# Kernel tuning notes

Measured on AMD Instinct MI355X. Metric: run time of the kernel, lower is better.

The kernel has to match this reference:

```python
import jax, jax.numpy as jnp
import numpy as np

N, D, R, E = 10000, 1024, 8, 80000


def setup_inputs() -> dict:
    key = jax.random.key(0)
    ks = jax.random.split(key, 8)
    s = 1.0 / np.sqrt(D)
    x = jax.random.normal(ks[0], (N, D), dtype=jnp.float32)
    edge_index = jax.random.randint(ks[1], (2, E), 0, N, dtype=jnp.int64)
    edge_type = jax.random.randint(ks[2], (E,), 0, R, dtype=jnp.int64)
    weight = jax.random.normal(ks[3], (R, D, D), dtype=jnp.float32) * s  # per-relation W_r
    root = jax.random.normal(ks[4], (D, D), dtype=jnp.float32) * s      # root/self-loop weight
    bias = jnp.zeros((D,), dtype=jnp.float32)
    w_gate = jax.random.normal(ks[5], (2 * D, D), dtype=jnp.float32) * (1.0 / np.sqrt(2 * D))
    b_gate = jnp.zeros((D,), dtype=jnp.float32)
    return {"x": x, "edge_index": edge_index, "edge_type": edge_type,
            "weight": weight, "root": root, "bias": bias,
            "w_gate": w_gate, "b_gate": b_gate}


def _rgcn(x, edge_index, edge_type, weight, root, bias):
    # PyG RGCNConv (aggr='mean'): per relation r, mean-aggregate x[src] into dst,
    # then transform by W_r (aggregate-then-transform, equivalent by linearity).
    src, dst = edge_index[0], edge_index[1]
    msgs = x[src]                                   # [E, D] gather
    out = x @ root + bias                           # root/self connection
    n = x.shape[0]
    for r in range(weight.shape[0]):                # small fixed relation loop
        mask = (edge_type == r).astype(x.dtype)     # [E]
        sums = jax.ops.segment_sum(msgs * mask[:, None], dst, num_segments=n)
        cnt = jax.ops.segment_sum(mask, dst, num_segments=n)
        mean = sums / jnp.maximum(cnt, 1.0)[:, None]
        out = out + mean @ weight[r]
    return out


def reference(x, edge_index, edge_type, weight, root, bias, w_gate, b_gate):
    u = _rgcn(x, edge_index, edge_type, weight, root, bias)
    # dropout p=0 -> identity
    z = jnp.concatenate([u, x], axis=1) @ w_gate + b_gate
    h = jnp.tanh(u) * z + x * (1.0 - z)
    return h
```

## Files before the change

### kernel.cpp

```cpp
#include <hip/hip_runtime.h>
#include <math.h>

typedef unsigned short u16;
typedef __attribute__((ext_vector_type(8))) short bf16x8;
typedef __attribute__((ext_vector_type(4))) float f32x4;

static constexpr int kN = 10000;
static constexpr int kNpad = 10240;
static constexpr int kD = 1024;
static constexpr int kR = 8;
static constexpr int kE = 80000;
static constexpr int kKz = 2 * kD;
static constexpr int kCrows = kNpad * (kR + 1);
static constexpr int kTilesY1 = kCrows / 128;

#define GLB(p) ((const __attribute__((address_space(1))) unsigned int*)(const void*)(p))
#define LDSP(p) ((__attribute__((address_space(3))) unsigned int*)(p))

__device__ __forceinline__ u16 f2bf(float f) {
    union { float f; unsigned int i; } c; c.f = f;
    unsigned int u = c.i;
    return (u16)((u + 0x7FFFu + ((u >> 16) & 1u)) >> 16);
}
__device__ __forceinline__ float bf2f(u16 u) {
    union { unsigned int i; float f; } c; c.i = ((unsigned int)u) << 16;
    return c.f;
}
__device__ __forceinline__ ushort4 f2bf4(float4 v) {
    ushort4 o; o.x = f2bf(v.x); o.y = f2bf(v.y); o.z = f2bf(v.z); o.w = f2bf(v.w);
    return o;
}

__global__ void zero16(uint4* __restrict__ p, long n16) {
    long i = (long)blockIdx.x * blockDim.x + threadIdx.x;
    long st = (long)gridDim.x * blockDim.x;
    uint4 z = make_uint4(0, 0, 0, 0);
    for (; i < n16; i += st) p[i] = z;
}

__global__ void mark_edges(const int* __restrict__ src, const int* __restrict__ dst,
                           const int* __restrict__ etype,
                           int* __restrict__ cntd, int* __restrict__ flag) {
    int e = blockIdx.x * blockDim.x + threadIdx.x;
    if (e < kE) {
        atomicAdd(&cntd[dst[e]], 1);
        flag[etype[e] * kN + src[e]] = 1;
    }
}

__global__ __launch_bounds__(1024) void scan_rowptr(const int* __restrict__ cnt,
                                                    int* __restrict__ rowptr,
                                                    int* __restrict__ cursor) {
    __shared__ int wsum[16];
    __shared__ int carry;
    const int tid = threadIdx.x;
    const int lane = tid & 63;
    const int w = tid >> 6;
    if (tid == 0) carry = 0;
    const int nchunk = (kN + 1024) / 1024;
    for (int ch = 0; ch < nchunk; ++ch) {
        int idx = ch * 1024 + tid;
        int v = (idx < kN) ? cnt[idx] : 0;
        int s = v;
#pragma unroll
        for (int off = 1; off < 64; off <<= 1) {
            int t = __shfl_up(s, off, 64);
            if (lane >= off) s += t;
        }
        if (lane == 63) wsum[w] = s;
        __syncthreads();
        if (w == 0 && lane < 16) {
            int t = wsum[lane];
#pragma unroll
            for (int off = 1; off < 16; off <<= 1) {
                int tt = __shfl_up(t, off, 64);
                if (lane >= off) t += tt;
            }
            wsum[lane] = t;
        }
        __syncthreads();
        int wpre = (w > 0) ? wsum[w - 1] : 0;
        int incl = s + wpre + carry;
        int excl = incl - v;
        if (idx <= kN) rowptr[idx] = excl;
        if (idx < kN) cursor[idx] = 0;
        __syncthreads();
        if (tid == 1023) carry = incl;
        __syncthreads();
    }
}

__global__ __launch_bounds__(1024) void compact_scan(const int* __restrict__ flag,
                                                     int* __restrict__ row_src,
                                                     int* __restrict__ pos_tab,
                                                     int* __restrict__ relcnt9) {
    const int tid = threadIdx.x;
    if (blockIdx.x == kR) {
        for (int i = tid; i < kNpad; i += 1024) row_src[i] = i;
        if (tid == 0) relcnt9[0] = kN;
        return;
    }
    const int r = blockIdx.x;
    const int base = kNpad * (r + 1);
    __shared__ int wsum[16];
    __shared__ int carry;
    const int lane = tid & 63;
    const int w = tid >> 6;
    if (tid == 0) carry = 0;
    const int nchunk = (kN + 1023) / 1024;
    for (int ch = 0; ch < nchunk; ++ch) {
        int idx = ch * 1024 + tid;
        int v = (idx < kN) ? flag[r * kN + idx] : 0;
        int s = v;
#pragma unroll
        for (int off = 1; off < 64; off <<= 1) {
            int t = __shfl_up(s, off, 64);
            if (lane >= off) s += t;
        }
        if (lane == 63) wsum[w] = s;
        __syncthreads();
        if (w == 0 && lane < 16) {
            int t = wsum[lane];
#pragma unroll
            for (int off = 1; off < 16; off <<= 1) {
                int tt = __shfl_up(t, off, 64);
                if (lane >= off) t += tt;
            }
            wsum[lane] = t;
        }
        __syncthreads();
        int wpre = (w > 0) ? wsum[w - 1] : 0;
        int incl = s + wpre + carry;
        int excl = incl - v;
        if (idx < kN && v) {
            row_src[base + excl] = idx;
            pos_tab[r * kN + idx] = base + excl;
        }
        __syncthreads();
        if (tid == 1023) carry = incl;
        __syncthreads();
    }
    if (tid == 0) relcnt9[r + 1] = carry;
}

__global__ void fill_edges(const int* __restrict__ src, const int* __restrict__ dst,
                           const int* __restrict__ etype, const int* __restrict__ rowptr,
                           int* __restrict__ cursor, const int* __restrict__ pos_tab,
                           int* __restrict__ erec) {
    int e = blockIdx.x * blockDim.x + threadIdx.x;
    if (e < kE) {
        int d = dst[e], r = etype[e], s = src[e];
        int pos = rowptr[d] + atomicAdd(&cursor[d], 1);
        erec[pos] = (pos_tab[r * kN + s] << 3) | r;
    }
}

__global__ void cvt_x(const float* __restrict__ x, u16* __restrict__ ga) {
    int row = blockIdx.x;
    int c = threadIdx.x << 2;
    float4 v = *reinterpret_cast<const float4*>(x + (size_t)row * kD + c);
    *reinterpret_cast<ushort4*>(ga + (size_t)row * kKz + kD + c) = f2bf4(v);
}

__global__ void transpose_to_bf16(const float* __restrict__ S, u16* __restrict__ D,
                                  int rows, int cols, int ldD) {
    S += (size_t)blockIdx.z * rows * cols;
    D += (size_t)blockIdx.z * rows * cols;
    __shared__ float t[32][33];
    int c0 = blockIdx.x * 32, r0 = blockIdx.y * 32;
    int x = threadIdx.x, y = threadIdx.y;
#pragma unroll
    for (int i = 0; i < 32; i += 8)
        t[y + i][x] = S[(size_t)(r0 + y + i) * cols + c0 + x];
    __syncthreads();
#pragma unroll
    for (int i = 0; i < 32; i += 8)
        D[(size_t)(c0 + y + i) * ldD + r0 + x] = f2bf(t[x][y + i]);
}

__global__ __launch_bounds__(256) void aggregate(const u16* __restrict__ yc,
                                                 const float* __restrict__ bias,
                                                 const int* __restrict__ rowptr,
                                                 const int* __restrict__ erec,
                                                 u16* __restrict__ ga) {
    const int d = blockIdx.x;
    const int c = threadIdx.x << 2;
    const int e0 = rowptr[d], e1 = rowptr[d + 1];

    __shared__ float rs[kR];
    if (threadIdx.x == 0) {
        int cc[kR] = {0, 0, 0, 0, 0, 0, 0, 0};
        for (int e = e0; e < e1; ++e) cc[erec[e] & 7]++;
#pragma unroll
        for (int r = 0; r < kR; ++r) rs[r] = 1.0f / fmaxf((float)cc[r], 1.0f);
    }
    __syncthreads();

    ushort4 rv = *reinterpret_cast<const ushort4*>(yc + (size_t)d * kD + c);
    float4 bv = *reinterpret_cast<const float4*>(bias + c);
    float4 acc = make_float4(bf2f(rv.x) + bv.x, bf2f(rv.y) + bv.y,
                             bf2f(rv.z) + bv.z, bf2f(rv.w) + bv.w);

    int e = e0;
    for (; e + 1 < e1; e += 2) {
        int rec0 = erec[e];
        int rec1 = erec[e + 1];
        ushort4 v0 = *reinterpret_cast<const ushort4*>(yc + (size_t)(rec0 >> 3) * kD + c);
        ushort4 v1 = *reinterpret_cast<const ushort4*>(yc + (size_t)(rec1 >> 3) * kD + c);
        float s0 = rs[rec0 & 7];
        float s1 = rs[rec1 & 7];
        acc.x += s0 * bf2f(v0.x); acc.y += s0 * bf2f(v0.y);
        acc.z += s0 * bf2f(v0.z); acc.w += s0 * bf2f(v0.w);
        acc.x += s1 * bf2f(v1.x); acc.y += s1 * bf2f(v1.y);
        acc.z += s1 * bf2f(v1.z); acc.w += s1 * bf2f(v1.w);
    }
    if (e < e1) {
        int rec = erec[e];
        float sc = rs[rec & 7];
        ushort4 v = *reinterpret_cast<const ushort4*>(yc + (size_t)(rec >> 3) * kD + c);
        acc.x += sc * bf2f(v.x); acc.y += sc * bf2f(v.y);
        acc.z += sc * bf2f(v.z); acc.w += sc * bf2f(v.w);
    }
    *reinterpret_cast<ushort4*>(ga + (size_t)d * kKz + c) = f2bf4(acc);
}

__global__ __launch_bounds__(256, 3) void gemm_compact(
    const u16* __restrict__ xb, int ldx,
    const u16* __restrict__ Bt9,
    const int* __restrict__ row_src, const int* __restrict__ relcnt9,
    u16* __restrict__ yc)
{
    const int t = blockIdx.y;
    const int relidx = t / 80;
    const int lt = t - relidx * 80;
    if (lt * 128 >= relcnt9[relidx]) return;

    __shared__ u16 sA[2][128 * 32];
    __shared__ u16 sB[2][128 * 32];

    const int tid = threadIdx.x;
    const int wave = tid >> 6;
    const int lane = tid & 63;

    const int row0 = t * 128;
    const int col0 = blockIdx.x * 128;

    const int srow = wave * 16 + (lane >> 2);
    const int scol = (lane & 3) * 8;

    const u16* gA0 = xb + (size_t)row_src[row0 + srow] * ldx + scol;
    const u16* gA1 = xb + (size_t)row_src[row0 + 64 + srow] * ldx + scol;
    const u16* gB0 = Bt9 + (size_t)(relidx * kD + col0 + srow) * kD + scol;
    const u16* gB1 = Bt9 + (size_t)(relidx * kD + col0 + 64 + srow) * kD + scol;

    const int lofA0 = (wave * 16) * 32;
    const int lofA1 = (64 + wave * 16) * 32;

    const int mq = (wave >> 1) * 64;
    const int nq = (wave & 1) * 64;
    const int fm = lane & 15;
    const int fk = (lane >> 4) * 8;

    f32x4 zf = {0.0f, 0.0f, 0.0f, 0.0f};
    f32x4 acc[4][4];
#pragma unroll
    for (int i = 0; i < 4; ++i)
#pragma unroll
        for (int j = 0; j < 4; ++j) acc[i][j] = zf;

    __builtin_amdgcn_global_load_lds(GLB(gA0), LDSP(sA[0] + lofA0), 16, 0, 0);
    __builtin_amdgcn_global_load_lds(GLB(gA1), LDSP(sA[0] + lofA1), 16, 0, 0);
    __builtin_amdgcn_global_load_lds(GLB(gB0), LDSP(sB[0] + lofA0), 16, 0, 0);
    __builtin_amdgcn_global_load_lds(GLB(gB1), LDSP(sB[0] + lofA1), 16, 0, 0);
    gA0 += 32; gA1 += 32; gB0 += 32; gB1 += 32;
    __syncthreads();

    int cur = 0;
    for (int k0 = 0; k0 < kD; k0 += 32) {
        if (k0 + 32 < kD) {
            u16* dA = sA[cur ^ 1];
            u16* dB = sB[cur ^ 1];
            __builtin_amdgcn_global_load_lds(GLB(gA0), LDSP(dA + lofA0), 16, 0, 0);
            __builtin_amdgcn_global_load_lds(GLB(gA1), LDSP(dA + lofA1), 16, 0, 0);
            __builtin_amdgcn_global_load_lds(GLB(gB0), LDSP(dB + lofA0), 16, 0, 0);
            __builtin_amdgcn_global_load_lds(GLB(gB1), LDSP(dB + lofA1), 16, 0, 0);
            gA0 += 32; gA1 += 32; gB0 += 32; gB1 += 32;
        }

        const u16* cA = sA[cur];
        const u16* cB = sB[cur];
        bf16x8 af[4], bfr[4];
#pragma unroll
        for (int i = 0; i < 4; ++i)
            af[i] = *reinterpret_cast<const bf16x8*>(&cA[(mq + i * 16 + fm) * 32 + fk]);
#pragma unroll
        for (int j = 0; j < 4; ++j)
            bfr[j] = *reinterpret_cast<const bf16x8*>(&cB[(nq + j * 16 + fm) * 32 + fk]);
#pragma unroll
        for (int i = 0; i < 4; ++i)
#pragma unroll
            for (int j = 0; j < 4; ++j)
                acc[i][j] = __builtin_amdgcn_mfma_f32_16x16x32_bf16(bfr[j], af[i], acc[i][j], 0, 0, 0);

        __syncthreads();
        cur ^= 1;
    }

    const int cq = (lane >> 4) * 4;
#pragma unroll
    for (int i = 0; i < 4; ++i) {
        int row = row0 + mq + i * 16 + fm;
#pragma unroll
        for (int j = 0; j < 4; ++j) {
            int col = col0 + nq + j * 16 + cq;
            f32x4 v = acc[i][j];
            ushort4 o;
            o.x = f2bf(v[0]); o.y = f2bf(v[1]); o.z = f2bf(v[2]); o.w = f2bf(v[3]);
            *reinterpret_cast<ushort4*>(yc + (size_t)row * kD + col) = o;
        }
    }
}

__global__ __launch_bounds__(256, 3) void gemm_mfma_gate(
    const u16* __restrict__ A, int lda,
    const u16* __restrict__ Bt, int ldb, int K,
    int M, const float* __restrict__ bias,
    float* __restrict__ Cf, const u16* __restrict__ uga, const float* __restrict__ xo)
{
    __shared__ u16 sA[2][128 * 32];
    __shared__ u16 sB[2][128 * 32];

    const int tid = threadIdx.x;
    const int wave = tid >> 6;
    const int lane = tid & 63;

    constexpr int GX = kD / 128;
    constexpr int GY = kNpad / 128;
    const int lin = blockIdx.y * GX + blockIdx.x;
    const int xcd = lin & 7;
    const int pos = lin >> 3;
    const int ty = xcd * (GY / 8) + (pos >> 3);
    const int tx = pos & 7;

    const int row0 = ty * 128;
    const int col0 = tx * 128;

    const int srow = wave * 16 + (lane >> 2);
    const int scol = (lane & 3) * 8;

    const u16* gA0 = A + (size_t)(row0 + srow) * lda + scol;
    const u16* gA1 = A + (size_t)(row0 + 64 + srow) * lda + scol;
    const u16* gB0 = Bt + (size_t)(col0 + srow) * ldb + scol;
    const u16* gB1 = Bt + (size_t)(col0 + 64 + srow) * ldb + scol;

    const int lof0 = (wave * 16) * 32;
    const int lof1 = (64 + wave * 16) * 32;

    const int mq = (wave >> 1) * 64;
    const int nq = (wave & 1) * 64;
    const int fm = lane & 15;
    const int fk = (lane >> 4) * 8;

    f32x4 zf = {0.0f, 0.0f, 0.0f, 0.0f};
    f32x4 acc[4][4];
#pragma unroll
    for (int i = 0; i < 4; ++i)
#pragma unroll
        for (int j = 0; j < 4; ++j) acc[i][j] = zf;

    __builtin_amdgcn_global_load_lds(GLB(gA0), LDSP(sA[0] + lof0), 16, 0, 0);
    __builtin_amdgcn_global_load_lds(GLB(gA1), LDSP(sA[0] + lof1), 16, 0, 0);
    __builtin_amdgcn_global_load_lds(GLB(gB0), LDSP(sB[0] + lof0), 16, 0, 0);
    __builtin_amdgcn_global_load_lds(GLB(gB1), LDSP(sB[0] + lof1), 16, 0, 0);
    gA0 += 32; gA1 += 32; gB0 += 32; gB1 += 32;
    __syncthreads();

    int cur = 0;
    for (int k0 = 0; k0 < K; k0 += 32) {
        if (k0 + 32 < K) {
            u16* dA = sA[cur ^ 1];
            u16* dB = sB[cur ^ 1];
            __builtin_amdgcn_global_load_lds(GLB(gA0), LDSP(dA + lof0), 16, 0, 0);
            __builtin_amdgcn_global_load_lds(GLB(gA1), LDSP(dA + lof1), 16, 0, 0);
            __builtin_amdgcn_global_load_lds(GLB(gB0), LDSP(dB + lof0), 16, 0, 0);
            __builtin_amdgcn_global_load_lds(GLB(gB1), LDSP(dB + lof1), 16, 0, 0);
            gA0 += 32; gA1 += 32; gB0 += 32; gB1 += 32;
        }

        const u16* cA = sA[cur];
        const u16* cB = sB[cur];
        bf16x8 af[4], bfr[4];
#pragma unroll
        for (int i = 0; i < 4; ++i)
            af[i] = *reinterpret_cast<const bf16x8*>(&cA[(mq + i * 16 + fm) * 32 + fk]);
#pragma unroll
        for (int j = 0; j < 4; ++j)
            bfr[j] = *reinterpret_cast<const bf16x8*>(&cB[(nq + j * 16 + fm) * 32 + fk]);
#pragma unroll
        for (int i = 0; i < 4; ++i)
#pragma unroll
            for (int j = 0; j < 4; ++j)
                acc[i][j] = __builtin_amdgcn_mfma_f32_16x16x32_bf16(bfr[j], af[i], acc[i][j], 0, 0, 0);

        __syncthreads();
        cur ^= 1;
    }

    const int cq = (lane >> 4) * 4;
#pragma unroll
    for (int i = 0; i < 4; ++i) {
        int row = row0 + mq + i * 16 + fm;
        if (row >= M) continue;
#pragma unroll
        for (int j = 0; j < 4; ++j) {
            int col = col0 + nq + j * 16 + cq;
            f32x4 v = acc[i][j];
            float4 bv = *reinterpret_cast<const float4*>(bias + col);
            v[0] += bv.x; v[1] += bv.y; v[2] += bv.z; v[3] += bv.w;
            ushort4 ur = *reinterpret_cast<const ushort4*>(uga + (size_t)row * kKz + col);
            float4 xr = *reinterpret_cast<const float4*>(xo + (size_t)row * kD + col);
            float4 h;
            h.x = tanhf(bf2f(ur.x)) * v[0] + xr.x * (1.0f - v[0]);
            h.y = tanhf(bf2f(ur.y)) * v[1] + xr.y * (1.0f - v[1]);
            h.z = tanhf(bf2f(ur.z)) * v[2] + xr.z * (1.0f - v[2]);
            h.w = tanhf(bf2f(ur.w)) * v[3] + xr.w * (1.0f - v[3]);
            *reinterpret_cast<float4*>(Cf + (size_t)row * kD + col) = h;
        }
    }
}

extern "C" void kernel_launch(void* const* d_in, const int* in_sizes, int n_in,
                              void* d_out, int out_size, void* d_ws, size_t ws_size,
                              hipStream_t stream) {
    (void)in_sizes; (void)n_in; (void)out_size; (void)ws_size;

    const float* x     = (const float*)d_in[0];
    const int* eidx    = (const int*)d_in[1];
    const int* etype   = (const int*)d_in[2];
    const float* weight= (const float*)d_in[3];
    const float* root  = (const float*)d_in[4];
    const float* bias  = (const float*)d_in[5];
    const float* wgate = (const float*)d_in[6];
    const float* bgate = (const float*)d_in[7];
    float* out = (float*)d_out;

    const int* src = eidx;
    const int* dst = eidx + kE;

    char* ws = (char*)d_ws;
    size_t off = 0;
    u16* yc   = (u16*)(ws + off);    off += (size_t)kCrows * kD * 2;
    u16* ga   = (u16*)(ws + off);    off += (size_t)kNpad * kKz * 2;
    u16* Bt9  = (u16*)(ws + off);    off += (size_t)(kR + 1) * kD * kD * 2;
    u16* wg_t = (u16*)(ws + off);    off += (size_t)kD * kKz * 2;
    int* cntd    = (int*)(ws + off); off += (size_t)kN * 4;
    int* flag    = (int*)(ws + off); off += (size_t)kR * kN * 4;
    int* row_src = (int*)(ws + off); off += (size_t)kCrows * 4;
    int* pos_tab = (int*)(ws + off); off += (size_t)kR * kN * 4;
    int* rowp    = (int*)(ws + off); off += (size_t)(kN + 16) * 4;
    int* curs    = (int*)(ws + off); off += (size_t)kN * 4;
    int* erec    = (int*)(ws + off); off += (size_t)kE * 4;
    int* relcnt9 = (int*)(ws + off); off += 16 * 4;

    zero16<<<180, 256, 0, stream>>>((uint4*)cntd, (long)(kN + kR * kN + kCrows) / 4);

    mark_edges<<<(kE + 255) / 256, 256, 0, stream>>>(src, dst, etype, cntd, flag);
    scan_rowptr<<<1, 1024, 0, stream>>>(cntd, rowp, curs);
    compact_scan<<<kR + 1, 1024, 0, stream>>>(flag, row_src, pos_tab, relcnt9);
    fill_edges<<<(kE + 255) / 256, 256, 0, stream>>>(src, dst, etype, rowp, curs,
                                                     pos_tab, erec);

    zero16<<<256, 256, 0, stream>>>((uint4*)(ga + (size_t)kN * kKz),
                                    (long)(kNpad - kN) * kKz * 2 / 16);

    cvt_x<<<kN, 256, 0, stream>>>(x, ga);

    {
        dim3 b(32, 8);
        transpose_to_bf16<<<dim3(kD / 32, kD / 32, 1), b, 0, stream>>>(root, Bt9, kD, kD, kD);
        transpose_to_bf16<<<dim3(kD / 32, kD / 32, kR), b, 0, stream>>>(
            weight, Bt9 + (size_t)kD * kD, kD, kD, kD);
        transpose_to_bf16<<<dim3(kD / 32, kKz / 32, 1), b, 0, stream>>>(wgate, wg_t, kKz, kD, kKz);
    }

    dim3 g1(kD / 128, kTilesY1);
    gemm_compact<<<g1, 256, 0, stream>>>(ga + kD, kKz, Bt9, row_src, relcnt9, yc);

    aggregate<<<kN, 256, 0, stream>>>(yc, bias, rowp, erec, ga);

    dim3 g2(kD / 128, kNpad / 128);
    gemm_mfma_gate<<<g2, 256, 0, stream>>>(ga, kKz, wg_t, kKz, kKz, kN, bgate, out, ga, x);
}
```

Before: 478.2 us.

## Triple-buffer GEMM LDS staging with explicit vmcnt waits; unroll edge gather by four

```diff
diff --git a/kernel.cpp b/kernel.cpp
--- a/kernel.cpp
+++ b/kernel.cpp
@@ -202,19 +202,23 @@
                              bf2f(rv.z) + bv.z, bf2f(rv.w) + bv.w);
 
     int e = e0;
-    for (; e + 1 < e1; e += 2) {
-        int rec0 = erec[e];
-        int rec1 = erec[e + 1];
+    for (; e + 3 < e1; e += 4) {
+        int rec0 = erec[e], rec1 = erec[e + 1], rec2 = erec[e + 2], rec3 = erec[e + 3];
         ushort4 v0 = *reinterpret_cast<const ushort4*>(yc + (size_t)(rec0 >> 3) * kD + c);
         ushort4 v1 = *reinterpret_cast<const ushort4*>(yc + (size_t)(rec1 >> 3) * kD + c);
-        float s0 = rs[rec0 & 7];
-        float s1 = rs[rec1 & 7];
+        ushort4 v2 = *reinterpret_cast<const ushort4*>(yc + (size_t)(rec2 >> 3) * kD + c);
+        ushort4 v3 = *reinterpret_cast<const ushort4*>(yc + (size_t)(rec3 >> 3) * kD + c);
+        float s0 = rs[rec0 & 7], s1 = rs[rec1 & 7], s2 = rs[rec2 & 7], s3 = rs[rec3 & 7];
         acc.x += s0 * bf2f(v0.x); acc.y += s0 * bf2f(v0.y);
         acc.z += s0 * bf2f(v0.z); acc.w += s0 * bf2f(v0.w);
         acc.x += s1 * bf2f(v1.x); acc.y += s1 * bf2f(v1.y);
         acc.z += s1 * bf2f(v1.z); acc.w += s1 * bf2f(v1.w);
-    }
-    if (e < e1) {
+        acc.x += s2 * bf2f(v2.x); acc.y += s2 * bf2f(v2.y);
+        acc.z += s2 * bf2f(v2.z); acc.w += s2 * bf2f(v2.w);
+        acc.x += s3 * bf2f(v3.x); acc.y += s3 * bf2f(v3.y);
+        acc.z += s3 * bf2f(v3.z); acc.w += s3 * bf2f(v3.w);
+    }
+    for (; e < e1; ++e) {
         int rec = erec[e];
         float sc = rs[rec & 7];
         ushort4 v = *reinterpret_cast<const ushort4*>(yc + (size_t)(rec >> 3) * kD + c);
@@ -230,19 +234,19 @@
     const int* __restrict__ row_src, const int* __restrict__ relcnt9,
     u16* __restrict__ yc)
 {
-    const int t = blockIdx.y;
-    const int relidx = t / 80;
-    const int lt = t - relidx * 80;
+    const int t0 = blockIdx.y;
+    const int relidx = t0 / 80;
+    const int lt = t0 - relidx * 80;
     if (lt * 128 >= relcnt9[relidx]) return;
 
-    __shared__ u16 sA[2][128 * 32];
-    __shared__ u16 sB[2][128 * 32];
+    __shared__ u16 sA[3][128 * 32];
+    __shared__ u16 sB[3][128 * 32];
 
     const int tid = threadIdx.x;
     const int wave = tid >> 6;
     const int lane = tid & 63;
 
-    const int row0 = t * 128;
+    const int row0 = t0 * 128;
     const int col0 = blockIdx.x * 128;
 
     const int srow = wave * 16 + (lane >> 2);
@@ -253,8 +257,8 @@
     const u16* gB0 = Bt9 + (size_t)(relidx * kD + col0 + srow) * kD + scol;
     const u16* gB1 = Bt9 + (size_t)(relidx * kD + col0 + 64 + srow) * kD + scol;
 
-    const int lofA0 = (wave * 16) * 32;
-    const int lofA1 = (64 + wave * 16) * 32;
+    const int lof0 = (wave * 16) * 32;
+    const int lof1 = (64 + wave * 16) * 32;
 
     const int mq = (wave >> 1) * 64;
     const int nq = (wave & 1) * 64;
@@ -268,27 +272,33 @@
 #pragma unroll
         for (int j = 0; j < 4; ++j) acc[i][j] = zf;
 
-    __builtin_amdgcn_global_load_lds(GLB(gA0), LDSP(sA[0] + lofA0), 16, 0, 0);
-    __builtin_amdgcn_global_load_lds(GLB(gA1), LDSP(sA[0] + lofA1), 16, 0, 0);
-    __builtin_amdgcn_global_load_lds(GLB(gB0), LDSP(sB[0] + lofA0), 16, 0, 0);
-    __builtin_amdgcn_global_load_lds(GLB(gB1), LDSP(sB[0] + lofA1), 16, 0, 0);
-    gA0 += 32; gA1 += 32; gB0 += 32; gB1 += 32;
-    __syncthreads();
-
-    int cur = 0;
-    for (int k0 = 0; k0 < kD; k0 += 32) {
-        if (k0 + 32 < kD) {
-            u16* dA = sA[cur ^ 1];
-            u16* dB = sB[cur ^ 1];
-            __builtin_amdgcn_global_load_lds(GLB(gA0), LDSP(dA + lofA0), 16, 0, 0);
-            __builtin_amdgcn_global_load_lds(GLB(gA1), LDSP(dA + lofA1), 16, 0, 0);
-            __builtin_amdgcn_global_load_lds(GLB(gB0), LDSP(dB + lofA0), 16, 0, 0);
-            __builtin_amdgcn_global_load_lds(GLB(gB1), LDSP(dB + lofA1), 16, 0, 0);
-            gA0 += 32; gA1 += 32; gB0 += 32; gB1 += 32;
-        }
-
-        const u16* cA = sA[cur];
-        const u16* cB = sB[cur];
+    auto stage = [&](int s) {
+        __builtin_amdgcn_global_load_lds(GLB(gA0), LDSP(sA[s] + lof0), 16, 0, 0);
+        __builtin_amdgcn_global_load_lds(GLB(gA1), LDSP(sA[s] + lof1), 16, 0, 0);
+        __builtin_amdgcn_global_load_lds(GLB(gB0), LDSP(sB[s] + lof0), 16, 0, 0);
+        __builtin_amdgcn_global_load_lds(GLB(gB1), LDSP(sB[s] + lof1), 16, 0, 0);
+        gA0 += 32; gA1 += 32; gB0 += 32; gB1 += 32;
+    };
+
+    constexpr int T = kD / 32;
+    stage(0);
+    stage(1);
+
+    int s = 0;
+    for (int t = 0; t < T; ++t) {
+        if (t + 2 < T) {
+            stage(s == 0 ? 2 : (s - 1));
+            asm volatile("s_waitcnt vmcnt(8)" ::: "memory");
+        } else if (t + 1 < T) {
+            asm volatile("s_waitcnt vmcnt(4)" ::: "memory");
+        } else {
+            asm volatile("s_waitcnt vmcnt(0)" ::: "memory");
+        }
+        __builtin_amdgcn_s_barrier();
+        asm volatile("" ::: "memory");
+
+        const u16* cA = sA[s];
+        const u16* cB = sB[s];
         bf16x8 af[4], bfr[4];
 #pragma unroll
         for (int i = 0; i < 4; ++i)
@@ -302,8 +312,9 @@
             for (int j = 0; j < 4; ++j)
                 acc[i][j] = __builtin_amdgcn_mfma_f32_16x16x32_bf16(bfr[j], af[i], acc[i][j], 0, 0, 0);
 
-        __syncthreads();
-        cur ^= 1;
+        asm volatile("" ::: "memory");
+        __builtin_amdgcn_s_barrier();
+        s = (s == 2) ? 0 : (s + 1);
     }
 
     const int cq = (lane >> 4) * 4;
@@ -327,8 +338,8 @@
     int M, const float* __restrict__ bias,
     float* __restrict__ Cf, const u16* __restrict__ uga, const float* __restrict__ xo)
 {
-    __shared__ u16 sA[2][128 * 32];
-    __shared__ u16 sB[2][128 * 32];
+    __shared__ u16 sA[3][128 * 32];
+    __shared__ u16 sB[3][128 * 32];
 
     const int tid = threadIdx.x;
     const int wave = tid >> 6;
@@ -368,27 +379,33 @@
 #pragma unroll
         for (int j = 0; j < 4; ++j) acc[i][j] = zf;
 
-    __builtin_amdgcn_global_load_lds(GLB(gA0), LDSP(sA[0] + lof0), 16, 0, 0);
-    __builtin_amdgcn_global_load_lds(GLB(gA1), LDSP(sA[0] + lof1), 16, 0, 0);
-    __builtin_amdgcn_global_load_lds(GLB(gB0), LDSP(sB[0] + lof0), 16, 0, 0);
-    __builtin_amdgcn_global_load_lds(GLB(gB1), LDSP(sB[0] + lof1), 16, 0, 0);
-    gA0 += 32; gA1 += 32; gB0 += 32; gB1 += 32;
-    __syncthreads();
-
-    int cur = 0;
-    for (int k0 = 0; k0 < K; k0 += 32) {
-        if (k0 + 32 < K) {
-            u16* dA = sA[cur ^ 1];
-            u16* dB = sB[cur ^ 1];
-            __builtin_amdgcn_global_load_lds(GLB(gA0), LDSP(dA + lof0), 16, 0, 0);
-            __builtin_amdgcn_global_load_lds(GLB(gA1), LDSP(dA + lof1), 16, 0, 0);
-            __builtin_amdgcn_global_load_lds(GLB(gB0), LDSP(dB + lof0), 16, 0, 0);
-            __builtin_amdgcn_global_load_lds(GLB(gB1), LDSP(dB + lof1), 16, 0, 0);
-            gA0 += 32; gA1 += 32; gB0 += 32; gB1 += 32;
-        }
-
-        const u16* cA = sA[cur];
-        const u16* cB = sB[cur];
+    auto stage = [&](int s) {
+        __builtin_amdgcn_global_load_lds(GLB(gA0), LDSP(sA[s] + lof0), 16, 0, 0);
+        __builtin_amdgcn_global_load_lds(GLB(gA1), LDSP(sA[s] + lof1), 16, 0, 0);
+        __builtin_amdgcn_global_load_lds(GLB(gB0), LDSP(sB[s] + lof0), 16, 0, 0);
+        __builtin_amdgcn_global_load_lds(GLB(gB1), LDSP(sB[s] + lof1), 16, 0, 0);
+        gA0 += 32; gA1 += 32; gB0 += 32; gB1 += 32;
+    };
+
+    const int T = K >> 5;
+    stage(0);
+    stage(1);
+
+    int s = 0;
+    for (int t = 0; t < T; ++t) {
+        if (t + 2 < T) {
+            stage(s == 0 ? 2 : (s - 1));
+            asm volatile("s_waitcnt vmcnt(8)" ::: "memory");
+        } else if (t + 1 < T) {
+            asm volatile("s_waitcnt vmcnt(4)" ::: "memory");
+        } else {
+            asm volatile("s_waitcnt vmcnt(0)" ::: "memory");
+        }
+        __builtin_amdgcn_s_barrier();
+        asm volatile("" ::: "memory");
+
+        const u16* cA = sA[s];
+        const u16* cB = sB[s];
         bf16x8 af[4], bfr[4];
 #pragma unroll
         for (int i = 0; i < 4; ++i)
@@ -402,8 +419,9 @@
             for (int j = 0; j < 4; ++j)
                 acc[i][j] = __builtin_amdgcn_mfma_f32_16x16x32_bf16(bfr[j], af[i], acc[i][j], 0, 0, 0);
 
-        __syncthreads();
-        cur ^= 1;
+        asm volatile("" ::: "memory");
+        __builtin_amdgcn_s_barrier();
+        s = (s == 2) ? 0 : (s + 1);
     }
 
     const int cq = (lane >> 4) * 4;
```

Result: no change. 481.1 us (+0.6%).
